# Kernel tuning notes

Hardware: AMD Instinct MI355X
Metric: run time of the kernel (lower is better)

## Reference

```python
import jax, jax.numpy as jnp
import numpy as np

B, T, H = 32, 512, 512
NUM_LAYERS = 2  # outer modules; each nn.GRU itself has NUM_LAYERS internal layers
TOTAL = NUM_LAYERS * NUM_LAYERS  # 4 actual recurrent layers
EPS = 1e-5


def setup_inputs() -> dict:
    key = jax.random.key(0)
    ks = jax.random.split(key, 8)
    s = 1.0 / np.sqrt(H)
    x = jax.random.normal(ks[0], (B, T, H), dtype=jnp.float32)
    # descending lengths in [1, T] (enforce_sorted=True in torch)
    seq_lens = jnp.sort(jax.random.randint(ks[1], (B,), 1, T + 1))[::-1]
    Wih = jax.random.uniform(ks[2], (TOTAL, 3 * H, H), minval=-s, maxval=s)
    Whh = jax.random.uniform(ks[3], (TOTAL, 3 * H, H), minval=-s, maxval=s)
    bih = jax.random.uniform(ks[4], (TOTAL, 3 * H), minval=-s, maxval=s)
    bhh = jax.random.uniform(ks[5], (TOTAL, 3 * H), minval=-s, maxval=s)
    gamma = jnp.ones((NUM_LAYERS, H), jnp.float32)
    beta = jnp.zeros((NUM_LAYERS, H), jnp.float32)
    return {"x": x, "Wih": Wih, "Whh": Whh, "bih": bih, "bhh": bhh,
            "gamma": gamma, "beta": beta, "seq_lens": seq_lens}


def _gru_layer(x, wih, whh, bi, bh):
    # x: [B,T,I]; torch GRU equations (gate order r,z,n)
    xi = jnp.einsum('bti,gi->btg', x, wih) + bi  # [B,T,3H]

    def step(h, xt):
        hh = h @ whh.T + bh
        xr, xz, xn = jnp.split(xt, 3, axis=-1)
        hr, hz, hn = jnp.split(hh, 3, axis=-1)
        r = jax.nn.sigmoid(xr + hr)
        z = jax.nn.sigmoid(xz + hz)
        n = jnp.tanh(xn + r * hn)
        h = (1 - z) * n + z * h
        return h, h

    h0 = jnp.zeros((x.shape[0], whh.shape[1]), x.dtype)
    _, ys = jax.lax.scan(step, h0, jnp.swapaxes(xi, 0, 1))  # [T,B,H]
    return jnp.swapaxes(ys, 0, 1)


def _layernorm(x, g, b):
    mu = jnp.mean(x, axis=-1, keepdims=True)
    var = jnp.mean(jnp.square(x - mu), axis=-1, keepdims=True)
    return (x - mu) * jax.lax.rsqrt(var + EPS) * g + b


def reference(x, Wih, Whh, bih, bhh, gamma, beta, seq_lens):
    # pack_padded_sequence semantics (unidirectional): outputs at valid steps
    # t < len match the full-sequence run; padded steps become zeros after
    # pad_packed_sequence, then LayerNorm is applied to the whole padded tensor.
    mask = (jnp.arange(T)[None, :] < seq_lens[:, None])[:, :, None]  # [B,T,1]
    out = x
    idx = 0
    for l in range(NUM_LAYERS):
        for _k in range(NUM_LAYERS):  # each nn.GRU has NUM_LAYERS internal layers
            out = _gru_layer(out, Wih[idx], Whh[idx], bih[idx], bhh[idx])
            idx += 1
        out = jnp.where(mask, out, 0.0)
        out = _layernorm(out, gamma[l], beta[l])
    return out
```

## Files before the change

### kernel.cpp

```cpp
#include <hip/hip_runtime.h>

typedef unsigned short ushort_t;
typedef __attribute__((ext_vector_type(8))) short short8;
typedef __attribute__((ext_vector_type(4))) float f32x4;

#define B_ 32
#define T_ 512
#define H_ 512
#define CH_ 16

__device__ __forceinline__ float bf2f(ushort_t u) {
  union { unsigned int i; float f; } v; v.i = ((unsigned int)u) << 16; return v.f;
}
__device__ __forceinline__ ushort_t f2bf(float f) {
  union { float fv; unsigned int i; } v; v.fv = f;
  unsigned int x = v.i;
  x += 0x7fffu + ((x >> 16) & 1u);
  return (ushort_t)(x >> 16);
}

__device__ __forceinline__ float fsig(float a) {
  return __builtin_amdgcn_rcpf(1.f + __expf(-a));
}
__device__ __forceinline__ float ftanh(float a) {
  return 1.f - 2.f * __builtin_amdgcn_rcpf(1.f + __expf(2.f * a));
}

__device__ __forceinline__ void cload16(short8& dst, const ushort_t* p) {
  asm volatile("global_load_dwordx4 %0, %1, off sc0 sc1"
               : "=v"(dst) : "v"(p) : "memory");
}
__device__ __forceinline__ void cstore16(const short8& v, ushort_t* p) {
  asm volatile("global_store_dwordx4 %1, %0, off sc0 sc1"
               :: "v"(v), "v"(p) : "memory");
}
#define WAIT_VM0 asm volatile("s_waitcnt vmcnt(0)" ::: "memory")
__device__ __forceinline__ void vfence(short8& v) { asm volatile("" : "+v"(v)); }

__device__ __forceinline__ void poll_row(const int* row, int nf) {
  const int lane = threadIdx.x & 63;
  if (nf > 64) {
    for (;;) {
      int a = __hip_atomic_load(row + lane,      __ATOMIC_RELAXED, __HIP_MEMORY_SCOPE_AGENT);
      int b = __hip_atomic_load(row + 64 + lane, __ATOMIC_RELAXED, __HIP_MEMORY_SCOPE_AGENT);
      if (__all(a != 0 && b != 0)) break;
      __builtin_amdgcn_s_sleep(1);
    }
  } else {
    for (;;) {
      int a = (lane < nf)
            ? __hip_atomic_load(row + lane, __ATOMIC_RELAXED, __HIP_MEMORY_SCOPE_AGENT) : 1;
      if (__all(a != 0)) break;
      __builtin_amdgcn_s_sleep(1);
    }
  }
  asm volatile("" ::: "memory");
}

__global__ void prep_w(const float* __restrict__ Wih, const float* __restrict__ Whh,
                       ushort_t* __restrict__ WihBf, ushort_t* __restrict__ WhhBf) {
  int i = blockIdx.x * 256 + threadIdx.x;
  WihBf[i] = f2bf(Wih[i]);
  WhhBf[i] = f2bf(Whh[i]);
}
__global__ void prep_x(const float* __restrict__ x, ushort_t* __restrict__ xA) {
  int i = blockIdx.x * 256 + threadIdx.x;
  int h  = i & (H_ - 1);
  int tb = i >> 9;
  int b  = tb & (B_ - 1);
  int t  = tb >> 5;
  xA[i] = f2bf(x[((size_t)b * T_ + t) * H_ + h]);
}

__device__ void gru_stage(
    const ushort_t* __restrict__ xin, ushort_t* __restrict__ xout,
    const ushort_t* __restrict__ Wih, const ushort_t* __restrict__ Whh,
    const float* __restrict__ bih, const float* __restrict__ bhh,
    ushort_t* __restrict__ hbuf,
    int* __restrict__ selfFl,
    const int* __restrict__ prodFl,
    int prodN, int wg,
    float (*Gbuf)[2][48][33])
{
  const int tid   = threadIdx.x;
  const int lane  = tid & 63;
  const int wave  = tid >> 6;
  const int jb    = wg * CH_;
  const int m16   = lane & 15;
  const int quad  = lane >> 4;
  const int bcol  = (wave & 1) * 16 + m16;

  const ushort_t* Wsel = (wave < 2) ? Wih : Whh;
  short8 afrag[3][16];
#pragma unroll
  for (int g = 0; g < 3; ++g) {
    const ushort_t* wp = Wsel + (size_t)(g * H_ + jb + m16) * H_ + quad * 8;
#pragma unroll
    for (int kk = 0; kk < 16; ++kk)
      afrag[g][kk] = *(const short8*)(wp + kk * 32);
  }

  const int b0 = tid & 31;
  const int c  = tid >> 5;
  const int c0 = 2 * c, c1 = 2 * c + 1;
  const float bxr0 = bih[0*H_ + jb + c0], bhr0 = bhh[0*H_ + jb + c0];
  const float bxz0 = bih[1*H_ + jb + c0], bhz0 = bhh[1*H_ + jb + c0];
  const float bxn0 = bih[2*H_ + jb + c0], bhn0 = bhh[2*H_ + jb + c0];
  const float bxr1 = bih[0*H_ + jb + c1], bhr1 = bhh[0*H_ + jb + c1];
  const float bxz1 = bih[1*H_ + jb + c1], bhz1 = bhh[1*H_ + jb + c1];
  const float bxn1 = bih[2*H_ + jb + c1], bhn1 = bhh[2*H_ + jb + c1];
  float hp0 = 0.f, hp1 = 0.f;

  for (int s = 0; s < T_; ++s) {
    const int p = s & 1;
    f32x4 acc0 = {0.f, 0.f, 0.f, 0.f};
    f32x4 acc1 = acc0, acc2 = acc0;

    if (wave < 2) {
      const ushort_t* src = xin + ((size_t)s * B_ + bcol) * H_ + quad * 8;
      if (prodFl) {
        poll_row(prodFl + s * prodN, prodN);
        short8 bfr[16];
#pragma unroll
        for (int kk = 0; kk < 16; ++kk) cload16(bfr[kk], src + kk * 32);
        WAIT_VM0;
#pragma unroll
        for (int kk = 0; kk < 16; ++kk) {
          vfence(bfr[kk]);
          acc0 = __builtin_amdgcn_mfma_f32_16x16x32_bf16(afrag[0][kk], bfr[kk], acc0, 0, 0, 0);
          acc1 = __builtin_amdgcn_mfma_f32_16x16x32_bf16(afrag[1][kk], bfr[kk], acc1, 0, 0, 0);
          acc2 = __builtin_amdgcn_mfma_f32_16x16x32_bf16(afrag[2][kk], bfr[kk], acc2, 0, 0, 0);
        }
      } else {
#pragma unroll
        for (int kk = 0; kk < 16; ++kk) {
          short8 bf = *(const short8*)(src + kk * 32);
          acc0 = __builtin_amdgcn_mfma_f32_16x16x32_bf16(afrag[0][kk], bf, acc0, 0, 0, 0);
          acc1 = __builtin_amdgcn_mfma_f32_16x16x32_bf16(afrag[1][kk], bf, acc1, 0, 0, 0);
          acc2 = __builtin_amdgcn_mfma_f32_16x16x32_bf16(afrag[2][kk], bf, acc2, 0, 0, 0);
        }
      }
    } else {
      if (s > 0) poll_row(selfFl + (s - 1) * 128, 128);
      const ushort_t* src = hbuf + ((size_t)p * B_ + bcol) * H_ + quad * 8;
      short8 bfr[16];
#pragma unroll
      for (int kk = 0; kk < 16; ++kk) cload16(bfr[kk], src + kk * 32);
      WAIT_VM0;
#pragma unroll
      for (int kk = 0; kk < 16; ++kk) {
        vfence(bfr[kk]);
        acc0 = __builtin_amdgcn_mfma_f32_16x16x32_bf16(afrag[0][kk], bfr[kk], acc0, 0, 0, 0);
        acc1 = __builtin_amdgcn_mfma_f32_16x16x32_bf16(afrag[1][kk], bfr[kk], acc1, 0, 0, 0);
        acc2 = __builtin_amdgcn_mfma_f32_16x16x32_bf16(afrag[2][kk], bfr[kk], acc2, 0, 0, 0);
      }
    }

    float (*Gd)[33] = Gbuf[p][(wave < 2) ? 0 : 1];
#pragma unroll
    for (int r = 0; r < 4; ++r) {
      Gd[ 0 + quad * 4 + r][bcol] = acc0[r];
      Gd[16 + quad * 4 + r][bcol] = acc1[r];
      Gd[32 + quad * 4 + r][bcol] = acc2[r];
    }
    __syncthreads();

    float (*Gx)[33] = Gbuf[p][0];
    float (*Gh)[33] = Gbuf[p][1];
    ushort_t* hdst = hbuf + (size_t)(p ^ 1) * B_ * H_;
    {
      float rr = fsig(Gx[c0][b0] + bxr0 + Gh[c0][b0] + bhr0);
      float zz = fsig(Gx[16 + c0][b0] + bxz0 + Gh[16 + c0][b0] + bhz0);
      float nn = ftanh(Gx[32 + c0][b0] + bxn0 + rr * (Gh[32 + c0][b0] + bhn0));
      hp0 = (1.f - zz) * nn + zz * hp0;
    }
    {
      float rr = fsig(Gx[c1][b0] + bxr1 + Gh[c1][b0] + bhr1);
      float zz = fsig(Gx[16 + c1][b0] + bxz1 + Gh[16 + c1][b0] + bhz1);
      float nn = ftanh(Gx[32 + c1][b0] + bxn1 + rr * (Gh[32 + c1][b0] + bhn1));
      hp1 = (1.f - zz) * nn + zz * hp1;
    }
    unsigned int pack = (unsigned int)f2bf(hp0) | ((unsigned int)f2bf(hp1) << 16);
    __hip_atomic_store((unsigned int*)(hdst + (size_t)b0 * H_ + jb + c0), pack,
                       __ATOMIC_RELAXED, __HIP_MEMORY_SCOPE_AGENT);
    __hip_atomic_store((unsigned int*)(xout + ((size_t)s * B_ + b0) * H_ + jb + c0), pack,
                       __ATOMIC_RELAXED, __HIP_MEMORY_SCOPE_AGENT);

    WAIT_VM0;
    if (lane == 0)
      __hip_atomic_store(selfFl + s * 128 + wg * 4 + wave, 1,
                         __ATOMIC_RELAXED, __HIP_MEMORY_SCOPE_AGENT);
  }
}

__device__ void ln_stage(
    const ushort_t* __restrict__ xin,
    ushort_t* __restrict__ xout_bf,
    float* __restrict__ out_f32,
    const float* __restrict__ gamma, const float* __restrict__ beta,
    const int* __restrict__ seq,
    int* __restrict__ selfFl,
    const int* __restrict__ prodFl, int prodN, int wg)
{
  const int lane = threadIdx.x & 63;
  const int wv   = threadIdx.x >> 6;
  const int b    = wg * 4 + wv;
  const int len  = seq[b];
  const int h0   = lane * 8;

  float g[8], be[8];
#pragma unroll
  for (int j = 0; j < 8; ++j) { g[j] = gamma[h0 + j]; be[j] = beta[h0 + j]; }

  for (int s = 0; s < T_; ++s) {
    poll_row(prodFl + s * prodN, prodN);
    short8 raw;
    cload16(raw, xin + ((size_t)s * B_ + b) * H_ + h0);
    WAIT_VM0;
    vfence(raw);
    const bool valid = s < len;
    float v[8];
#pragma unroll
    for (int j = 0; j < 8; ++j) v[j] = valid ? bf2f((ushort_t)raw[j]) : 0.f;

    float sum = 0.f, sq = 0.f;
#pragma unroll
    for (int j = 0; j < 8; ++j) { sum += v[j]; sq += v[j] * v[j]; }
#pragma unroll
    for (int off = 32; off > 0; off >>= 1) {
      sum += __shfl_xor(sum, off);
      sq  += __shfl_xor(sq, off);
    }
    float mu   = sum * (1.f / H_);
    float var  = sq * (1.f / H_) - mu * mu;
    float rstd = rsqrtf(var + 1e-5f);

    if (xout_bf) {
      short8 o;
#pragma unroll
      for (int j = 0; j < 8; ++j)
        o[j] = (short)f2bf((v[j] - mu) * rstd * g[j] + be[j]);
      cstore16(o, xout_bf + ((size_t)s * B_ + b) * H_ + h0);
      WAIT_VM0;
      if (lane == 0)
        __hip_atomic_store(selfFl + s * 32 + b, 1,
                           __ATOMIC_RELAXED, __HIP_MEMORY_SCOPE_AGENT);
    } else {
      float* dst = out_f32 + ((size_t)b * T_ + s) * H_ + h0;
#pragma unroll
      for (int j = 0; j < 8; ++j)
        dst[j] = (v[j] - mu) * rstd * g[j] + be[j];
    }
  }
}

__global__ __launch_bounds__(256, 1) void gru_mega(
    ushort_t* __restrict__ xA, ushort_t* __restrict__ xB, ushort_t* __restrict__ xC,
    const ushort_t* __restrict__ WihBf, const ushort_t* __restrict__ WhhBf,
    const float* __restrict__ bih, const float* __restrict__ bhh,
    const float* __restrict__ gamma, const float* __restrict__ beta,
    const int* __restrict__ seq,
    ushort_t* __restrict__ hbase, int* __restrict__ flbase,
    float* __restrict__ out)
{
  __shared__ float Gbuf[2][2][48][33];

  const int bid = blockIdx.x;
  const int GRUF = T_ * 128;
  const int LNF  = T_ * 32;
  int* fl0   = flbase;
  int* fl1   = flbase + GRUF;
  int* flln0 = flbase + 2 * GRUF;
  int* fl2   = flbase + 2 * GRUF + LNF;
  int* fl3   = flbase + 3 * GRUF + LNF;
  const int WM  = 3 * H_ * H_;
  const int HBL = 2 * B_ * H_;

  if (bid < 32) {
    gru_stage(xA, xB, WihBf, WhhBf, bih, bhh,
              hbase, fl0, nullptr, 0, bid, Gbuf);
  } else if (bid < 64) {
    gru_stage(xB, xC, WihBf + WM, WhhBf + WM, bih + 1536, bhh + 1536,
              hbase + HBL, fl1, fl0, 128, bid - 32, Gbuf);
  } else if (bid < 72) {
    ln_stage(xC, xA, nullptr, gamma, beta, seq, flln0, fl1, 128, bid - 64);
  } else if (bid < 104) {
    gru_stage(xA, xC, WihBf + 2 * WM, WhhBf + 2 * WM, bih + 2 * 1536, bhh + 2 * 1536,
              hbase + 2 * HBL, fl2, flln0, 32, bid - 72, Gbuf);
  } else if (bid < 136) {
    gru_stage(xC, xB, WihBf + 3 * WM, WhhBf + 3 * WM, bih + 3 * 1536, bhh + 3 * 1536,
              hbase + 3 * HBL, fl3, fl2, 128, bid - 104, Gbuf);
  } else {
    ln_stage(xB, nullptr, out, gamma + H_, beta + H_, seq,
             nullptr, fl3, 128, bid - 136);
  }
}

#define WIH_OFF 0u
#define WHH_OFF 6291456u
#define XA_OFF  12582912u
#define XB_OFF  29360128u
#define XC_OFF  46137344u
#define HB_OFF  62914560u
#define FL_OFF  63176704u

extern "C" void kernel_launch(void* const* d_in, const int* in_sizes, int n_in,
                              void* d_out, int out_size, void* d_ws, size_t ws_size,
                              hipStream_t stream) {
  (void)in_sizes; (void)n_in; (void)out_size; (void)ws_size;
  const float* x     = (const float*)d_in[0];
  const float* Wih   = (const float*)d_in[1];
  const float* Whh   = (const float*)d_in[2];
  const float* bih   = (const float*)d_in[3];
  const float* bhh   = (const float*)d_in[4];
  const float* gamma = (const float*)d_in[5];
  const float* beta  = (const float*)d_in[6];
  const int*   seq   = (const int*)d_in[7];

  char* ws = (char*)d_ws;
  ushort_t* WihBf = (ushort_t*)(ws + WIH_OFF);
  ushort_t* WhhBf = (ushort_t*)(ws + WHH_OFF);
  ushort_t* xA    = (ushort_t*)(ws + XA_OFF);
  ushort_t* xB    = (ushort_t*)(ws + XB_OFF);
  ushort_t* xC    = (ushort_t*)(ws + XC_OFF);
  ushort_t* hbase = (ushort_t*)(ws + HB_OFF);
  int*      flags = (int*)(ws + FL_OFF);

  hipMemsetAsync(ws + HB_OFF, 0, 262144u + 1114112u, stream);

  prep_w<<<3145728 / 256, 256, 0, stream>>>(Wih, Whh, WihBf, WhhBf);
  prep_x<<<8388608 / 256, 256, 0, stream>>>(x, xA);

  gru_mega<<<144, 256, 0, stream>>>(xA, xB, xC, WihBf, WhhBf,
                                    bih, bhh, gamma, beta, seq,
                                    hbase, flags, (float*)d_out);
}
```

Measured before the change: 3.891 ms.

## Tag hidden-state words with step index and tile activations per workgroup

Each hidden-state value is stored as a 32-bit word carrying the bf16 value plus a step tag. Consumers spin-read the h buffer until every tag reaches the current step, so the recurrent wait no longer depends only on flag arrays plus a full store fence. Activations are re-laid out in per-workgroup 16-column tiles so MFMA operand loads are contiguous, and separate x/h flag arrays let flags be published with partial vmcnt waits instead of vmcnt(0). This adds doubled h traffic and a polling loop over 32 loads per step, and the still-present hFl poll may cancel part of the latency saved.

Result: slower. 4.537 ms (+16.6%).

```diff
diff --git a/kernel.cpp b/kernel.cpp
--- a/kernel.cpp
+++ b/kernel.cpp
@@ -1,13 +1,15 @@
 #include <hip/hip_runtime.h>
 
 typedef unsigned short ushort_t;
+typedef unsigned int uint_t;
 typedef __attribute__((ext_vector_type(8))) short short8;
 typedef __attribute__((ext_vector_type(4))) float f32x4;
+typedef __attribute__((ext_vector_type(4))) unsigned int u32x4;
 
 #define B_ 32
 #define T_ 512
 #define H_ 512
-#define CH_ 16
+#define XT_ 16384
 
 __device__ __forceinline__ float bf2f(ushort_t u) {
   union { unsigned int i; float f; } v; v.i = ((unsigned int)u) << 16; return v.f;
@@ -18,6 +20,7 @@
   x += 0x7fffu + ((x >> 16) & 1u);
   return (ushort_t)(x >> 16);
 }
+__device__ __forceinline__ uint_t umin_(uint_t a, uint_t b) { return a < b ? a : b; }
 
 __device__ __forceinline__ float fsig(float a) {
   return __builtin_amdgcn_rcpf(1.f + __expf(-a));
@@ -26,15 +29,24 @@
   return 1.f - 2.f * __builtin_amdgcn_rcpf(1.f + __expf(2.f * a));
 }
 
-__device__ __forceinline__ void cload16(short8& dst, const ushort_t* p) {
-  asm volatile("global_load_dwordx4 %0, %1, off sc0 sc1"
-               : "=v"(dst) : "v"(p) : "memory");
+__device__ __forceinline__ void cload16(short8& d, const ushort_t* p) {
+  asm volatile("global_load_dwordx4 %0, %1, off sc0 sc1" : "=v"(d) : "v"(p) : "memory");
+}
+__device__ __forceinline__ void cload16u(u32x4& d, const uint_t* p) {
+  asm volatile("global_load_dwordx4 %0, %1, off sc0 sc1" : "=v"(d) : "v"(p) : "memory");
 }
 __device__ __forceinline__ void cstore16(const short8& v, ushort_t* p) {
-  asm volatile("global_store_dwordx4 %1, %0, off sc0 sc1"
-               :: "v"(v), "v"(p) : "memory");
+  asm volatile("global_store_dwordx4 %1, %0, off sc0 sc1" :: "v"(v), "v"(p) : "memory");
+}
+__device__ __forceinline__ void cstore8(unsigned long long v, uint_t* p) {
+  asm volatile("global_store_dwordx2 %1, %0, off sc0 sc1" :: "v"(v), "v"(p) : "memory");
+}
+__device__ __forceinline__ void cstore4(uint_t v, ushort_t* p) {
+  asm volatile("global_store_dword %1, %0, off sc0 sc1" :: "v"(v), "v"(p) : "memory");
 }
 #define WAIT_VM0 asm volatile("s_waitcnt vmcnt(0)" ::: "memory")
+#define WAIT_VM1 asm volatile("s_waitcnt vmcnt(1)" ::: "memory")
+#define WAIT_VM3 asm volatile("s_waitcnt vmcnt(3)" ::: "memory")
 __device__ __forceinline__ void vfence(short8& v) { asm volatile("" : "+v"(v)); }
 
 __device__ __forceinline__ void poll_row(const int* row, int nf) {
@@ -65,19 +77,20 @@
 }
 __global__ void prep_x(const float* __restrict__ x, ushort_t* __restrict__ xA) {
   int i = blockIdx.x * 256 + threadIdx.x;
-  int h  = i & (H_ - 1);
-  int tb = i >> 9;
-  int b  = tb & (B_ - 1);
-  int t  = tb >> 5;
-  xA[i] = f2bf(x[((size_t)b * T_ + t) * H_ + h]);
+  int ch = i & 15;
+  int b  = (i >> 4) & 31;
+  int wg = (i >> 9) & 31;
+  int t  = i >> 14;
+  xA[i] = f2bf(x[((size_t)b * T_ + t) * H_ + wg * 16 + ch]);
 }
 
 __device__ void gru_stage(
     const ushort_t* __restrict__ xin, ushort_t* __restrict__ xout,
     const ushort_t* __restrict__ Wih, const ushort_t* __restrict__ Whh,
     const float* __restrict__ bih, const float* __restrict__ bhh,
-    ushort_t* __restrict__ hbuf,
-    int* __restrict__ selfFl,
+    uint_t* __restrict__ hT,
+    int* __restrict__ xFl,
+    int* __restrict__ hFl,
     const int* __restrict__ prodFl,
     int prodN, int wg,
     float (*Gbuf)[2][48][33])
@@ -85,7 +98,7 @@
   const int tid   = threadIdx.x;
   const int lane  = tid & 63;
   const int wave  = tid >> 6;
-  const int jb    = wg * CH_;
+  const int jb    = wg * 16;
   const int m16   = lane & 15;
   const int quad  = lane >> 4;
   const int bcol  = (wave & 1) * 16 + m16;
@@ -100,9 +113,9 @@
       afrag[g][kk] = *(const short8*)(wp + kk * 32);
   }
 
-  const int b0 = tid & 31;
-  const int c  = tid >> 5;
-  const int c0 = 2 * c, c1 = 2 * c + 1;
+  const int b0 = tid >> 3;
+  const int c8 = tid & 7;
+  const int c0 = 2 * c8, c1 = c0 + 1;
   const float bxr0 = bih[0*H_ + jb + c0], bhr0 = bhh[0*H_ + jb + c0];
   const float bxz0 = bih[1*H_ + jb + c0], bhz0 = bhh[1*H_ + jb + c0];
   const float bxn0 = bih[2*H_ + jb + c0], bhn0 = bhh[2*H_ + jb + c0];
@@ -111,18 +124,21 @@
   const float bxn1 = bih[2*H_ + jb + c1], bhn1 = bhh[2*H_ + jb + c1];
   float hp0 = 0.f, hp1 = 0.f;
 
+  const int xoff = (quad >> 1) * 512 + bcol * 16 + (quad & 1) * 8;
+  const uint_t* hb = hT + (quad >> 1) * 512 + bcol * 16 + (quad & 1) * 8;
+
   for (int s = 0; s < T_; ++s) {
     const int p = s & 1;
     f32x4 acc0 = {0.f, 0.f, 0.f, 0.f};
     f32x4 acc1 = acc0, acc2 = acc0;
 
     if (wave < 2) {
-      const ushort_t* src = xin + ((size_t)s * B_ + bcol) * H_ + quad * 8;
+      const ushort_t* src = xin + (size_t)s * XT_ + xoff;
       if (prodFl) {
         poll_row(prodFl + s * prodN, prodN);
         short8 bfr[16];
 #pragma unroll
-        for (int kk = 0; kk < 16; ++kk) cload16(bfr[kk], src + kk * 32);
+        for (int kk = 0; kk < 16; ++kk) cload16(bfr[kk], src + kk * 1024);
         WAIT_VM0;
 #pragma unroll
         for (int kk = 0; kk < 16; ++kk) {
@@ -134,25 +150,39 @@
       } else {
 #pragma unroll
         for (int kk = 0; kk < 16; ++kk) {
-          short8 bf = *(const short8*)(src + kk * 32);
+          short8 bf = *(const short8*)(src + kk * 1024);
           acc0 = __builtin_amdgcn_mfma_f32_16x16x32_bf16(afrag[0][kk], bf, acc0, 0, 0, 0);
           acc1 = __builtin_amdgcn_mfma_f32_16x16x32_bf16(afrag[1][kk], bf, acc1, 0, 0, 0);
           acc2 = __builtin_amdgcn_mfma_f32_16x16x32_bf16(afrag[2][kk], bf, acc2, 0, 0, 0);
         }
       }
-    } else {
-      if (s > 0) poll_row(selfFl + (s - 1) * 128, 128);
-      const ushort_t* src = hbuf + ((size_t)p * B_ + bcol) * H_ + quad * 8;
-      short8 bfr[16];
-#pragma unroll
-      for (int kk = 0; kk < 16; ++kk) cload16(bfr[kk], src + kk * 32);
-      WAIT_VM0;
+    } else if (s > 0) {
+      poll_row(hFl + (s - 1) * 128, 128);
+      const uint_t* hsrc = hb + p * 16384;
+      const uint_t tgt = ((uint_t)s) << 16;
+      u32x4 t[32];
+      for (;;) {
+#pragma unroll
+        for (int i = 0; i < 32; ++i)
+          cload16u(t[i], hsrc + (i >> 1) * 1024 + (i & 1) * 4);
+        WAIT_VM0;
+        uint_t m = 0xffffffffu;
+#pragma unroll
+        for (int i = 0; i < 32; ++i)
+          m = umin_(m, umin_(umin_(t[i].x, t[i].y), umin_(t[i].z, t[i].w)));
+        if (__all(m >= tgt)) break;
+        __builtin_amdgcn_s_sleep(2);
+      }
 #pragma unroll
       for (int kk = 0; kk < 16; ++kk) {
-        vfence(bfr[kk]);
-        acc0 = __builtin_amdgcn_mfma_f32_16x16x32_bf16(afrag[0][kk], bfr[kk], acc0, 0, 0, 0);
-        acc1 = __builtin_amdgcn_mfma_f32_16x16x32_bf16(afrag[1][kk], bfr[kk], acc1, 0, 0, 0);
-        acc2 = __builtin_amdgcn_mfma_f32_16x16x32_bf16(afrag[2][kk], bfr[kk], acc2, 0, 0, 0);
+        union { uint_t w[4]; short8 v; } u;
+        u.w[0] = __builtin_amdgcn_perm(t[2*kk].y,   t[2*kk].x,   0x05040100u);
+        u.w[1] = __builtin_amdgcn_perm(t[2*kk].w,   t[2*kk].z,   0x05040100u);
+        u.w[2] = __builtin_amdgcn_perm(t[2*kk+1].y, t[2*kk+1].x, 0x05040100u);
+        u.w[3] = __builtin_amdgcn_perm(t[2*kk+1].w, t[2*kk+1].z, 0x05040100u);
+        acc0 = __builtin_amdgcn_mfma_f32_16x16x32_bf16(afrag[0][kk], u.v, acc0, 0, 0, 0);
+        acc1 = __builtin_amdgcn_mfma_f32_16x16x32_bf16(afrag[1][kk], u.v, acc1, 0, 0, 0);
+        acc2 = __builtin_amdgcn_mfma_f32_16x16x32_bf16(afrag[2][kk], u.v, acc2, 0, 0, 0);
       }
     }
 
@@ -167,7 +197,6 @@
 
     float (*Gx)[33] = Gbuf[p][0];
     float (*Gh)[33] = Gbuf[p][1];
-    ushort_t* hdst = hbuf + (size_t)(p ^ 1) * B_ * H_;
     {
       float rr = fsig(Gx[c0][b0] + bxr0 + Gh[c0][b0] + bhr0);
       float zz = fsig(Gx[16 + c0][b0] + bxz0 + Gh[16 + c0][b0] + bhz0);
@@ -180,17 +209,24 @@
       float nn = ftanh(Gx[32 + c1][b0] + bxn1 + rr * (Gh[32 + c1][b0] + bhn1));
       hp1 = (1.f - zz) * nn + zz * hp1;
     }
-    unsigned int pack = (unsigned int)f2bf(hp0) | ((unsigned int)f2bf(hp1) << 16);
-    __hip_atomic_store((unsigned int*)(hdst + (size_t)b0 * H_ + jb + c0), pack,
+    const uint_t tagv = (uint_t)(s + 1);
+    uint_t v0 = (uint_t)f2bf(hp0), v1 = (uint_t)f2bf(hp1);
+    unsigned long long hw = (unsigned long long)(v0 | (tagv << 16))
+                          | ((unsigned long long)(v1 | (tagv << 16)) << 32);
+    cstore8(hw, hT + ((s + 1) & 1) * 16384 + wg * 512 + b0 * 16 + c0);
+    cstore4(v0 | (v1 << 16), xout + (size_t)s * XT_ + wg * 512 + b0 * 16 + c0);
+    if (lane == 0)
+      __hip_atomic_store(hFl + s * 128 + wg * 4 + wave, 1,
+                         __ATOMIC_RELAXED, __HIP_MEMORY_SCOPE_AGENT);
+    WAIT_VM3;
+    if (s > 0 && lane == 0)
+      __hip_atomic_store(xFl + (s - 1) * 128 + wg * 4 + wave, 1,
+                         __ATOMIC_RELAXED, __HIP_MEMORY_SCOPE_AGENT);
+  }
+  WAIT_VM0;
+  if (lane == 0)
+    __hip_atomic_store(xFl + (T_ - 1) * 128 + wg * 4 + wave, 1,
                        __ATOMIC_RELAXED, __HIP_MEMORY_SCOPE_AGENT);
-    __hip_atomic_store((unsigned int*)(xout + ((size_t)s * B_ + b0) * H_ + jb + c0), pack,
-                       __ATOMIC_RELAXED, __HIP_MEMORY_SCOPE_AGENT);
-
-    WAIT_VM0;
-    if (lane == 0)
-      __hip_atomic_store(selfFl + s * 128 + wg * 4 + wave, 1,
-                         __ATOMIC_RELAXED, __HIP_MEMORY_SCOPE_AGENT);
-  }
 }
 
 __device__ void ln_stage(
@@ -206,6 +242,7 @@
   const int wv   = threadIdx.x >> 6;
   const int b    = wg * 4 + wv;
   const int len  = seq[b];
+  const int off  = (lane >> 1) * 512 + b * 16 + (lane & 1) * 8;
   const int h0   = lane * 8;
 
   float g[8], be[8];
@@ -215,7 +252,7 @@
   for (int s = 0; s < T_; ++s) {
     poll_row(prodFl + s * prodN, prodN);
     short8 raw;
-    cload16(raw, xin + ((size_t)s * B_ + b) * H_ + h0);
+    cload16(raw, xin + (size_t)s * XT_ + off);
     WAIT_VM0;
     vfence(raw);
     const bool valid = s < len;
@@ -227,23 +264,23 @@
 #pragma unroll
     for (int j = 0; j < 8; ++j) { sum += v[j]; sq += v[j] * v[j]; }
 #pragma unroll
-    for (int off = 32; off > 0; off >>= 1) {
-      sum += __shfl_xor(sum, off);
-      sq  += __shfl_xor(sq, off);
+    for (int o = 32; o > 0; o >>= 1) {
+      sum += __shfl_xor(sum, o);
+      sq  += __shfl_xor(sq, o);
     }
     float mu   = sum * (1.f / H_);
     float var  = sq * (1.f / H_) - mu * mu;
     float rstd = rsqrtf(var + 1e-5f);
 
     if (xout_bf) {
-      short8 o;
+      short8 o8;
 #pragma unroll
       for (int j = 0; j < 8; ++j)
-        o[j] = (short)f2bf((v[j] - mu) * rstd * g[j] + be[j]);
-      cstore16(o, xout_bf + ((size_t)s * B_ + b) * H_ + h0);
-      WAIT_VM0;
-      if (lane == 0)
-        __hip_atomic_store(selfFl + s * 32 + b, 1,
+        o8[j] = (short)f2bf((v[j] - mu) * rstd * g[j] + be[j]);
+      cstore16(o8, xout_bf + (size_t)s * XT_ + off);
+      WAIT_VM1;
+      if (s > 0 && lane == 0)
+        __hip_atomic_store(selfFl + (s - 1) * 32 + b, 1,
                            __ATOMIC_RELAXED, __HIP_MEMORY_SCOPE_AGENT);
     } else {
       float* dst = out_f32 + ((size_t)b * T_ + s) * H_ + h0;
@@ -251,6 +288,12 @@
       for (int j = 0; j < 8; ++j)
         dst[j] = (v[j] - mu) * rstd * g[j] + be[j];
     }
+  }
+  if (xout_bf) {
+    WAIT_VM0;
+    if (lane == 0)
+      __hip_atomic_store(selfFl + (T_ - 1) * 32 + b, 1,
+                         __ATOMIC_RELAXED, __HIP_MEMORY_SCOPE_AGENT);
   }
 }
 
@@ -260,39 +303,38 @@
     const float* __restrict__ bih, const float* __restrict__ bhh,
     const float* __restrict__ gamma, const float* __restrict__ beta,
     const int* __restrict__ seq,
-    ushort_t* __restrict__ hbase, int* __restrict__ flbase,
+    uint_t* __restrict__ hTbase, int* __restrict__ xflbase,
+    int* __restrict__ hflbase, int* __restrict__ lnfl,
     float* __restrict__ out)
 {
   __shared__ float Gbuf[2][2][48][33];
 
   const int bid = blockIdx.x;
-  const int GRUF = T_ * 128;
-  const int LNF  = T_ * 32;
-  int* fl0   = flbase;
-  int* fl1   = flbase + GRUF;
-  int* flln0 = flbase + 2 * GRUF;
-  int* fl2   = flbase + 2 * GRUF + LNF;
-  int* fl3   = flbase + 3 * GRUF + LNF;
-  const int WM  = 3 * H_ * H_;
-  const int HBL = 2 * B_ * H_;
+  const int FS = T_ * 128;
+  const int WM = 3 * H_ * H_;
+  const int HTS = 2 * 32 * 32 * 16;
 
   if (bid < 32) {
     gru_stage(xA, xB, WihBf, WhhBf, bih, bhh,
-              hbase, fl0, nullptr, 0, bid, Gbuf);
+              hTbase, xflbase, hflbase, nullptr, 0, bid, Gbuf);
   } else if (bid < 64) {
     gru_stage(xB, xC, WihBf + WM, WhhBf + WM, bih + 1536, bhh + 1536,
-              hbase + HBL, fl1, fl0, 128, bid - 32, Gbuf);
+              hTbase + HTS, xflbase + FS, hflbase + FS,
+              xflbase, 128, bid - 32, Gbuf);
   } else if (bid < 72) {
-    ln_stage(xC, xA, nullptr, gamma, beta, seq, flln0, fl1, 128, bid - 64);
+    ln_stage(xC, xA, nullptr, gamma, beta, seq, lnfl,
+             xflbase + FS, 128, bid - 64);
   } else if (bid < 104) {
     gru_stage(xA, xC, WihBf + 2 * WM, WhhBf + 2 * WM, bih + 2 * 1536, bhh + 2 * 1536,
-              hbase + 2 * HBL, fl2, flln0, 32, bid - 72, Gbuf);
+              hTbase + 2 * HTS, xflbase + 2 * FS, hflbase + 2 * FS,
+              lnfl, 32, bid - 72, Gbuf);
   } else if (bid < 136) {
     gru_stage(xC, xB, WihBf + 3 * WM, WhhBf + 3 * WM, bih + 3 * 1536, bhh + 3 * 1536,
-              hbase + 3 * HBL, fl3, fl2, 128, bid - 104, Gbuf);
+              hTbase + 3 * HTS, xflbase + 3 * FS, hflbase + 3 * FS,
+              xflbase + 2 * FS, 128, bid - 104, Gbuf);
   } else {
     ln_stage(xB, nullptr, out, gamma + H_, beta + H_, seq,
-             nullptr, fl3, 128, bid - 136);
+             nullptr, xflbase + 3 * FS, 128, bid - 136);
   }
 }
 
@@ -301,8 +343,10 @@
 #define XA_OFF  12582912u
 #define XB_OFF  29360128u
 #define XC_OFF  46137344u
-#define HB_OFF  62914560u
-#define FL_OFF  63176704u
+#define HT_OFF  62914560u
+#define XFL_OFF 63438848u
+#define HFL_OFF 64487424u
+#define LNF_OFF 65536000u
 
 extern "C" void kernel_launch(void* const* d_in, const int* in_sizes, int n_in,
                               void* d_out, int out_size, void* d_ws, size_t ws_size,
@@ -323,15 +367,17 @@
   ushort_t* xA    = (ushort_t*)(ws + XA_OFF);
   ushort_t* xB    = (ushort_t*)(ws + XB_OFF);
   ushort_t* xC    = (ushort_t*)(ws + XC_OFF);
-  ushort_t* hbase = (ushort_t*)(ws + HB_OFF);
-  int*      flags = (int*)(ws + FL_OFF);
-
-  hipMemsetAsync(ws + HB_OFF, 0, 262144u + 1114112u, stream);
-
-  prep_w<<<3145728 / 256, 256, 0, stream>>>(Wih, Whh, WihBf, WhhBf);
-  prep_x<<<8388608 / 256, 256, 0, stream>>>(x, xA);
+  uint_t*   hT    = (uint_t*)(ws + HT_OFF);
+  int*      xfl   = (int*)(ws + XFL_OFF);
+  int*      hfl   = (int*)(ws + HFL_OFF);
+  int*      lnf   = (int*)(ws + LNF_OFF);
+
+  hipMemsetAsync(ws + HT_OFF, 0, 2686976u, stream);
+
+  prep_w<<<12288, 256, 0, stream>>>(Wih, Whh, WihBf, WhhBf);
+  prep_x<<<32768, 256, 0, stream>>>(x, xA);
 
   gru_mega<<<144, 256, 0, stream>>>(xA, xB, xC, WihBf, WhhBf,
                                     bih, bhh, gamma, beta, seq,
-                                    hbase, flags, (float*)d_out);
-}
+                                    hT, xfl, hfl, lnf, (float*)d_out);
+}
```

## Repartition GRU pipeline into 8 wide workgroups per layer with LDS-shared inputs

Applied to the files above, without the earlier changes.

Each GRU layer now runs on 8 workgroups of 1024 threads, each owning 64 hidden units, instead of 32 workgroups of 256 threads owning 16. Only one wave pair per input kind loads the x and h fragments from global memory and shares them through LDS, which cuts redundant global loads per step. Activations are stored in a blocked layout of 64-column tiles to match. Completion flags become bytes polled as packed dwords, and the LayerNorm stages interleave timesteps across two blocks. The cost is extra __syncthreads per step and a larger dynamic LDS footprint, and each block owns more of the per-step gate math.

Result: slower. 13.94 ms (+258.3%).

```diff
diff --git a/kernel.cpp b/kernel.cpp
--- a/kernel.cpp
+++ b/kernel.cpp
@@ -1,13 +1,15 @@
 #include <hip/hip_runtime.h>
 
 typedef unsigned short ushort_t;
+typedef unsigned int uint_t;
 typedef __attribute__((ext_vector_type(8))) short short8;
 typedef __attribute__((ext_vector_type(4))) float f32x4;
+typedef __attribute__((ext_vector_type(4))) float float4_t;
 
 #define B_ 32
 #define T_ 512
 #define H_ 512
-#define CH_ 16
+#define XT_ 16384
 
 __device__ __forceinline__ float bf2f(ushort_t u) {
   union { unsigned int i; float f; } v; v.i = ((unsigned int)u) << 16; return v.f;
@@ -26,33 +28,30 @@
   return 1.f - 2.f * __builtin_amdgcn_rcpf(1.f + __expf(2.f * a));
 }
 
-__device__ __forceinline__ void cload16(short8& dst, const ushort_t* p) {
-  asm volatile("global_load_dwordx4 %0, %1, off sc0 sc1"
-               : "=v"(dst) : "v"(p) : "memory");
+__device__ __forceinline__ void cload16(short8& d, const ushort_t* p) {
+  asm volatile("global_load_dwordx4 %0, %1, off sc0 sc1" : "=v"(d) : "v"(p) : "memory");
+}
+__device__ __forceinline__ void cstore4(uint_t v, ushort_t* p) {
+  asm volatile("global_store_dword %1, %0, off sc0 sc1" :: "v"(v), "v"(p) : "memory");
 }
 __device__ __forceinline__ void cstore16(const short8& v, ushort_t* p) {
-  asm volatile("global_store_dwordx4 %1, %0, off sc0 sc1"
-               :: "v"(v), "v"(p) : "memory");
+  asm volatile("global_store_dwordx4 %1, %0, off sc0 sc1" :: "v"(v), "v"(p) : "memory");
+}
+__device__ __forceinline__ void cstoreb(unsigned char* p) {
+  asm volatile("global_store_byte %0, %1, off sc0 sc1" :: "v"(p), "v"(1) : "memory");
 }
 #define WAIT_VM0 asm volatile("s_waitcnt vmcnt(0)" ::: "memory")
 __device__ __forceinline__ void vfence(short8& v) { asm volatile("" : "+v"(v)); }
 
-__device__ __forceinline__ void poll_row(const int* row, int nf) {
+__device__ __forceinline__ void poll_bytes(const unsigned char* row, int n4) {
   const int lane = threadIdx.x & 63;
-  if (nf > 64) {
-    for (;;) {
-      int a = __hip_atomic_load(row + lane,      __ATOMIC_RELAXED, __HIP_MEMORY_SCOPE_AGENT);
-      int b = __hip_atomic_load(row + 64 + lane, __ATOMIC_RELAXED, __HIP_MEMORY_SCOPE_AGENT);
-      if (__all(a != 0 && b != 0)) break;
-      __builtin_amdgcn_s_sleep(1);
-    }
-  } else {
-    for (;;) {
-      int a = (lane < nf)
-            ? __hip_atomic_load(row + lane, __ATOMIC_RELAXED, __HIP_MEMORY_SCOPE_AGENT) : 1;
-      if (__all(a != 0)) break;
-      __builtin_amdgcn_s_sleep(1);
-    }
+  const uint_t* r = (const uint_t*)row;
+  for (;;) {
+    uint_t a = (lane < n4)
+             ? __hip_atomic_load(r + lane, __ATOMIC_RELAXED, __HIP_MEMORY_SCOPE_AGENT)
+             : 0x01010101u;
+    if (__all(a == 0x01010101u)) break;
+    __builtin_amdgcn_s_sleep(1);
   }
   asm volatile("" ::: "memory");
 }
@@ -65,11 +64,11 @@
 }
 __global__ void prep_x(const float* __restrict__ x, ushort_t* __restrict__ xA) {
   int i = blockIdx.x * 256 + threadIdx.x;
-  int h  = i & (H_ - 1);
-  int tb = i >> 9;
-  int b  = tb & (B_ - 1);
-  int t  = tb >> 5;
-  xA[i] = f2bf(x[((size_t)b * T_ + t) * H_ + h]);
+  int ch = i & 63;
+  int b  = (i >> 6) & 31;
+  int wg = (i >> 11) & 7;
+  int t  = i >> 14;
+  xA[i] = f2bf(x[((size_t)b * T_ + t) * H_ + wg * 64 + ch]);
 }
 
 __device__ void gru_stage(
@@ -77,32 +76,39 @@
     const ushort_t* __restrict__ Wih, const ushort_t* __restrict__ Whh,
     const float* __restrict__ bih, const float* __restrict__ bhh,
     ushort_t* __restrict__ hbuf,
-    int* __restrict__ selfFl,
-    const int* __restrict__ prodFl,
-    int prodN, int wg,
-    float (*Gbuf)[2][48][33])
+    unsigned char* __restrict__ selfFl,
+    const unsigned char* __restrict__ inFl,
+    int inN4, int wg, char* lds)
 {
-  const int tid   = threadIdx.x;
-  const int lane  = tid & 63;
-  const int wave  = tid >> 6;
-  const int jb    = wg * CH_;
-  const int m16   = lane & 15;
-  const int quad  = lane >> 4;
-  const int bcol  = (wave & 1) * 16 + m16;
-
-  const ushort_t* Wsel = (wave < 2) ? Wih : Whh;
+  const int tid  = threadIdx.x;
+  const int lane = tid & 63;
+  const int wave = tid >> 6;
+  const int isH  = wave >> 3;
+  const int wl   = wave & 7;
+  const int ct   = wl >> 1, bh = wl & 1;
+  const bool loader = (ct == 0);
+  const int m16  = lane & 15, quad = lane >> 4;
+  const int jb   = wg * 64;
+
+  const ushort_t* Wsel = isH ? Whh : Wih;
   short8 afrag[3][16];
 #pragma unroll
   for (int g = 0; g < 3; ++g) {
-    const ushort_t* wp = Wsel + (size_t)(g * H_ + jb + m16) * H_ + quad * 8;
+    const ushort_t* wp = Wsel + (size_t)(g * H_ + jb + ct * 16 + m16) * H_ + quad * 8;
 #pragma unroll
     for (int kk = 0; kk < 16; ++kk)
       afrag[g][kk] = *(const short8*)(wp + kk * 32);
   }
 
-  const int b0 = tid & 31;
-  const int c  = tid >> 5;
-  const int c0 = 2 * c, c1 = 2 * c + 1;
+  char* stage = lds + isH * 32768;
+  float* Gx = (float*)(lds + 65536);
+  float* Gh = Gx + 192 * 33;
+  float* Gmine = isH ? Gh : Gx;
+  const int fragoff = (bh * 1024 + quad * 16 + m16) * 16;
+  const int colbase = (bh * 16 + m16) * 64 + quad * 8;
+
+  const int b0 = tid >> 5;
+  const int c0 = (tid & 31) * 2, c1 = c0 + 1;
   const float bxr0 = bih[0*H_ + jb + c0], bhr0 = bhh[0*H_ + jb + c0];
   const float bxz0 = bih[1*H_ + jb + c0], bhz0 = bhh[1*H_ + jb + c0];
   const float bxn0 = bih[2*H_ + jb + c0], bhn0 = bhh[2*H_ + jb + c0];
@@ -112,21 +118,47 @@
   float hp0 = 0.f, hp1 = 0.f;
 
   for (int s = 0; s < T_; ++s) {
-    const int p = s & 1;
     f32x4 acc0 = {0.f, 0.f, 0.f, 0.f};
     f32x4 acc1 = acc0, acc2 = acc0;
-
-    if (wave < 2) {
-      const ushort_t* src = xin + ((size_t)s * B_ + bcol) * H_ + quad * 8;
-      if (prodFl) {
-        poll_row(prodFl + s * prodN, prodN);
-        short8 bfr[16];
-#pragma unroll
-        for (int kk = 0; kk < 16; ++kk) cload16(bfr[kk], src + kk * 32);
+    short8 bfr[16];
+    const bool active = !isH || (s > 0);
+
+    if (active && loader) {
+      if (!isH) {
+        const ushort_t* src = xin + (size_t)s * XT_ + colbase;
+        if (inFl) {
+          poll_bytes(inFl + (size_t)s * inN4 * 4, inN4);
+#pragma unroll
+          for (int kk = 0; kk < 16; ++kk)
+            cload16(bfr[kk], src + (kk >> 1) * 2048 + (kk & 1) * 32);
+          WAIT_VM0;
+#pragma unroll
+          for (int kk = 0; kk < 16; ++kk) vfence(bfr[kk]);
+        } else {
+#pragma unroll
+          for (int kk = 0; kk < 16; ++kk)
+            bfr[kk] = *(const short8*)(src + (kk >> 1) * 2048 + (kk & 1) * 32);
+        }
+      } else {
+        poll_bytes(selfFl + (size_t)(s - 1) * 128, 32);
+        const ushort_t* src = hbuf + (size_t)(s & 1) * XT_ + colbase;
+#pragma unroll
+        for (int kk = 0; kk < 16; ++kk)
+          cload16(bfr[kk], src + (kk >> 1) * 2048 + (kk & 1) * 32);
         WAIT_VM0;
 #pragma unroll
+        for (int kk = 0; kk < 16; ++kk) vfence(bfr[kk]);
+      }
+#pragma unroll
+      for (int kk = 0; kk < 16; ++kk)
+        *(short8*)(stage + fragoff + kk * 1024) = bfr[kk];
+    }
+    __syncthreads();
+
+    if (active) {
+      if (loader) {
+#pragma unroll
         for (int kk = 0; kk < 16; ++kk) {
-          vfence(bfr[kk]);
           acc0 = __builtin_amdgcn_mfma_f32_16x16x32_bf16(afrag[0][kk], bfr[kk], acc0, 0, 0, 0);
           acc1 = __builtin_amdgcn_mfma_f32_16x16x32_bf16(afrag[1][kk], bfr[kk], acc1, 0, 0, 0);
           acc2 = __builtin_amdgcn_mfma_f32_16x16x32_bf16(afrag[2][kk], bfr[kk], acc2, 0, 0, 0);
@@ -134,62 +166,43 @@
       } else {
 #pragma unroll
         for (int kk = 0; kk < 16; ++kk) {
-          short8 bf = *(const short8*)(src + kk * 32);
-          acc0 = __builtin_amdgcn_mfma_f32_16x16x32_bf16(afrag[0][kk], bf, acc0, 0, 0, 0);
-          acc1 = __builtin_amdgcn_mfma_f32_16x16x32_bf16(afrag[1][kk], bf, acc1, 0, 0, 0);
-          acc2 = __builtin_amdgcn_mfma_f32_16x16x32_bf16(afrag[2][kk], bf, acc2, 0, 0, 0);
+          short8 fr = *(const short8*)(stage + fragoff + kk * 1024);
+          acc0 = __builtin_amdgcn_mfma_f32_16x16x32_bf16(afrag[0][kk], fr, acc0, 0, 0, 0);
+          acc1 = __builtin_amdgcn_mfma_f32_16x16x32_bf16(afrag[1][kk], fr, acc1, 0, 0, 0);
+          acc2 = __builtin_amdgcn_mfma_f32_16x16x32_bf16(afrag[2][kk], fr, acc2, 0, 0, 0);
         }
       }
-    } else {
-      if (s > 0) poll_row(selfFl + (s - 1) * 128, 128);
-      const ushort_t* src = hbuf + ((size_t)p * B_ + bcol) * H_ + quad * 8;
-      short8 bfr[16];
-#pragma unroll
-      for (int kk = 0; kk < 16; ++kk) cload16(bfr[kk], src + kk * 32);
-      WAIT_VM0;
-#pragma unroll
-      for (int kk = 0; kk < 16; ++kk) {
-        vfence(bfr[kk]);
-        acc0 = __builtin_amdgcn_mfma_f32_16x16x32_bf16(afrag[0][kk], bfr[kk], acc0, 0, 0, 0);
-        acc1 = __builtin_amdgcn_mfma_f32_16x16x32_bf16(afrag[1][kk], bfr[kk], acc1, 0, 0, 0);
-        acc2 = __builtin_amdgcn_mfma_f32_16x16x32_bf16(afrag[2][kk], bfr[kk], acc2, 0, 0, 0);
-      }
-    }
-
-    float (*Gd)[33] = Gbuf[p][(wave < 2) ? 0 : 1];
-#pragma unroll
-    for (int r = 0; r < 4; ++r) {
-      Gd[ 0 + quad * 4 + r][bcol] = acc0[r];
-      Gd[16 + quad * 4 + r][bcol] = acc1[r];
-      Gd[32 + quad * 4 + r][bcol] = acc2[r];
+    }
+
+    {
+      const int col = bh * 16 + m16;
+#pragma unroll
+      for (int r = 0; r < 4; ++r) {
+        Gmine[(  0 + ct * 16 + quad * 4 + r) * 33 + col] = acc0[r];
+        Gmine[( 64 + ct * 16 + quad * 4 + r) * 33 + col] = acc1[r];
+        Gmine[(128 + ct * 16 + quad * 4 + r) * 33 + col] = acc2[r];
+      }
     }
     __syncthreads();
 
-    float (*Gx)[33] = Gbuf[p][0];
-    float (*Gh)[33] = Gbuf[p][1];
-    ushort_t* hdst = hbuf + (size_t)(p ^ 1) * B_ * H_;
     {
-      float rr = fsig(Gx[c0][b0] + bxr0 + Gh[c0][b0] + bhr0);
-      float zz = fsig(Gx[16 + c0][b0] + bxz0 + Gh[16 + c0][b0] + bhz0);
-      float nn = ftanh(Gx[32 + c0][b0] + bxn0 + rr * (Gh[32 + c0][b0] + bhn0));
+      float rr = fsig(Gx[(  0 + c0) * 33 + b0] + bxr0 + Gh[(  0 + c0) * 33 + b0] + bhr0);
+      float zz = fsig(Gx[( 64 + c0) * 33 + b0] + bxz0 + Gh[( 64 + c0) * 33 + b0] + bhz0);
+      float nn = ftanh(Gx[(128 + c0) * 33 + b0] + bxn0 + rr * (Gh[(128 + c0) * 33 + b0] + bhn0));
       hp0 = (1.f - zz) * nn + zz * hp0;
     }
     {
-      float rr = fsig(Gx[c1][b0] + bxr1 + Gh[c1][b0] + bhr1);
-      float zz = fsig(Gx[16 + c1][b0] + bxz1 + Gh[16 + c1][b0] + bhz1);
-      float nn = ftanh(Gx[32 + c1][b0] + bxn1 + rr * (Gh[32 + c1][b0] + bhn1));
+      float rr = fsig(Gx[(  0 + c1) * 33 + b0] + bxr1 + Gh[(  0 + c1) * 33 + b0] + bhr1);
+      float zz = fsig(Gx[( 64 + c1) * 33 + b0] + bxz1 + Gh[( 64 + c1) * 33 + b0] + bhz1);
+      float nn = ftanh(Gx[(128 + c1) * 33 + b0] + bxn1 + rr * (Gh[(128 + c1) * 33 + b0] + bhn1));
       hp1 = (1.f - zz) * nn + zz * hp1;
     }
-    unsigned int pack = (unsigned int)f2bf(hp0) | ((unsigned int)f2bf(hp1) << 16);
-    __hip_atomic_store((unsigned int*)(hdst + (size_t)b0 * H_ + jb + c0), pack,
-                       __ATOMIC_RELAXED, __HIP_MEMORY_SCOPE_AGENT);
-    __hip_atomic_store((unsigned int*)(xout + ((size_t)s * B_ + b0) * H_ + jb + c0), pack,
-                       __ATOMIC_RELAXED, __HIP_MEMORY_SCOPE_AGENT);
-
+    uint_t pack = (uint_t)f2bf(hp0) | ((uint_t)f2bf(hp1) << 16);
+    cstore4(pack, hbuf + (size_t)((s + 1) & 1) * XT_ + wg * 2048 + b0 * 64 + c0);
+    cstore4(pack, xout + (size_t)s * XT_ + wg * 2048 + b0 * 64 + c0);
     WAIT_VM0;
     if (lane == 0)
-      __hip_atomic_store(selfFl + s * 128 + wg * 4 + wave, 1,
-                         __ATOMIC_RELAXED, __HIP_MEMORY_SCOPE_AGENT);
+      cstoreb(selfFl + (size_t)s * 128 + wg * 16 + wave);
   }
 }
 
@@ -199,100 +212,100 @@
     float* __restrict__ out_f32,
     const float* __restrict__ gamma, const float* __restrict__ beta,
     const int* __restrict__ seq,
-    int* __restrict__ selfFl,
-    const int* __restrict__ prodFl, int prodN, int wg)
+    unsigned char* __restrict__ selfFl,
+    const unsigned char* __restrict__ prodFl, int prodN4, int par)
 {
   const int lane = threadIdx.x & 63;
   const int wv   = threadIdx.x >> 6;
-  const int b    = wg * 4 + wv;
-  const int len  = seq[b];
-  const int h0   = lane * 8;
+  const int r0 = wv, r1 = wv + 16;
+  const int len0 = seq[r0], len1 = seq[r1];
+  const int off  = (lane >> 3) * 2048 + (lane & 7) * 8;
 
   float g[8], be[8];
 #pragma unroll
-  for (int j = 0; j < 8; ++j) { g[j] = gamma[h0 + j]; be[j] = beta[h0 + j]; }
-
-  for (int s = 0; s < T_; ++s) {
-    poll_row(prodFl + s * prodN, prodN);
-    short8 raw;
-    cload16(raw, xin + ((size_t)s * B_ + b) * H_ + h0);
+  for (int j = 0; j < 8; ++j) { g[j] = gamma[lane * 8 + j]; be[j] = beta[lane * 8 + j]; }
+
+  for (int s = par; s < T_; s += 2) {
+    poll_bytes(prodFl + (size_t)s * prodN4 * 4, prodN4);
+    short8 raw0, raw1;
+    cload16(raw0, xin + (size_t)s * XT_ + off + r0 * 64);
+    cload16(raw1, xin + (size_t)s * XT_ + off + r1 * 64);
     WAIT_VM0;
-    vfence(raw);
-    const bool valid = s < len;
-    float v[8];
-#pragma unroll
-    for (int j = 0; j < 8; ++j) v[j] = valid ? bf2f((ushort_t)raw[j]) : 0.f;
-
-    float sum = 0.f, sq = 0.f;
-#pragma unroll
-    for (int j = 0; j < 8; ++j) { sum += v[j]; sq += v[j] * v[j]; }
-#pragma unroll
-    for (int off = 32; off > 0; off >>= 1) {
-      sum += __shfl_xor(sum, off);
-      sq  += __shfl_xor(sq, off);
-    }
-    float mu   = sum * (1.f / H_);
-    float var  = sq * (1.f / H_) - mu * mu;
-    float rstd = rsqrtf(var + 1e-5f);
-
-    if (xout_bf) {
-      short8 o;
-#pragma unroll
-      for (int j = 0; j < 8; ++j)
-        o[j] = (short)f2bf((v[j] - mu) * rstd * g[j] + be[j]);
-      cstore16(o, xout_bf + ((size_t)s * B_ + b) * H_ + h0);
+    vfence(raw0); vfence(raw1);
+
+#pragma unroll
+    for (int rr = 0; rr < 2; ++rr) {
+      const short8& raw = rr ? raw1 : raw0;
+      const int r = rr ? r1 : r0;
+      const bool valid = s < (rr ? len1 : len0);
+      float v[8];
+#pragma unroll
+      for (int j = 0; j < 8; ++j) v[j] = valid ? bf2f((ushort_t)raw[j]) : 0.f;
+      float sum = 0.f, sq = 0.f;
+#pragma unroll
+      for (int j = 0; j < 8; ++j) { sum += v[j]; sq += v[j] * v[j]; }
+#pragma unroll
+      for (int o = 32; o > 0; o >>= 1) {
+        sum += __shfl_xor(sum, o);
+        sq  += __shfl_xor(sq, o);
+      }
+      float mu   = sum * (1.f / H_);
+      float var  = sq * (1.f / H_) - mu * mu;
+      float rstd = rsqrtf(var + 1e-5f);
+      if (xout_bf) {
+        short8 o8;
+#pragma unroll
+        for (int j = 0; j < 8; ++j)
+          o8[j] = (short)f2bf((v[j] - mu) * rstd * g[j] + be[j]);
+        cstore16(o8, xout_bf + (size_t)s * XT_ + off + r * 64);
+      } else {
+        float* dst = out_f32 + ((size_t)r * T_ + s) * H_ + lane * 8;
+        float4_t o4a, o4b;
+#pragma unroll
+        for (int j = 0; j < 4; ++j) o4a[j] = (v[j] - mu) * rstd * g[j] + be[j];
+#pragma unroll
+        for (int j = 0; j < 4; ++j) o4b[j] = (v[4 + j] - mu) * rstd * g[4 + j] + be[4 + j];
+        *(float4_t*)dst = o4a;
+        *(float4_t*)(dst + 4) = o4b;
+      }
+    }
+    if (selfFl) {
       WAIT_VM0;
-      if (lane == 0)
-        __hip_atomic_store(selfFl + s * 32 + b, 1,
-                           __ATOMIC_RELAXED, __HIP_MEMORY_SCOPE_AGENT);
-    } else {
-      float* dst = out_f32 + ((size_t)b * T_ + s) * H_ + h0;
-#pragma unroll
-      for (int j = 0; j < 8; ++j)
-        dst[j] = (v[j] - mu) * rstd * g[j] + be[j];
-    }
-  }
-}
-
-__global__ __launch_bounds__(256, 1) void gru_mega(
+      if (lane == 0) cstoreb(selfFl + (size_t)s * 16 + wv);
+    }
+  }
+}
+
+__global__ __launch_bounds__(1024) void gru_mega(
     ushort_t* __restrict__ xA, ushort_t* __restrict__ xB, ushort_t* __restrict__ xC,
     const ushort_t* __restrict__ WihBf, const ushort_t* __restrict__ WhhBf,
     const float* __restrict__ bih, const float* __restrict__ bhh,
     const float* __restrict__ gamma, const float* __restrict__ beta,
     const int* __restrict__ seq,
-    ushort_t* __restrict__ hbase, int* __restrict__ flbase,
-    float* __restrict__ out)
+    ushort_t* __restrict__ hbase, unsigned char* __restrict__ gfl,
+    unsigned char* __restrict__ lnfl, float* __restrict__ out)
 {
-  __shared__ float Gbuf[2][2][48][33];
-
+  extern __shared__ char lds[];
   const int bid = blockIdx.x;
-  const int GRUF = T_ * 128;
-  const int LNF  = T_ * 32;
-  int* fl0   = flbase;
-  int* fl1   = flbase + GRUF;
-  int* flln0 = flbase + 2 * GRUF;
-  int* fl2   = flbase + 2 * GRUF + LNF;
-  int* fl3   = flbase + 3 * GRUF + LNF;
-  const int WM  = 3 * H_ * H_;
-  const int HBL = 2 * B_ * H_;
+  const int WM = 3 * H_ * H_;
+  const int FL = T_ * 128;
 
   if (bid < 32) {
-    gru_stage(xA, xB, WihBf, WhhBf, bih, bhh,
-              hbase, fl0, nullptr, 0, bid, Gbuf);
-  } else if (bid < 64) {
-    gru_stage(xB, xC, WihBf + WM, WhhBf + WM, bih + 1536, bhh + 1536,
-              hbase + HBL, fl1, fl0, 128, bid - 32, Gbuf);
-  } else if (bid < 72) {
-    ln_stage(xC, xA, nullptr, gamma, beta, seq, flln0, fl1, 128, bid - 64);
-  } else if (bid < 104) {
-    gru_stage(xA, xC, WihBf + 2 * WM, WhhBf + 2 * WM, bih + 2 * 1536, bhh + 2 * 1536,
-              hbase + 2 * HBL, fl2, flln0, 32, bid - 72, Gbuf);
-  } else if (bid < 136) {
-    gru_stage(xC, xB, WihBf + 3 * WM, WhhBf + 3 * WM, bih + 3 * 1536, bhh + 3 * 1536,
-              hbase + 3 * HBL, fl3, fl2, 128, bid - 104, Gbuf);
+    const int layer = bid >> 3, wg = bid & 7;
+    const ushort_t* xi; ushort_t* xo;
+    const unsigned char* inFl; int inN4;
+    if (layer == 0)      { xi = xA; xo = xB; inFl = nullptr;      inN4 = 0;  }
+    else if (layer == 1) { xi = xB; xo = xC; inFl = gfl;          inN4 = 32; }
+    else if (layer == 2) { xi = xA; xo = xC; inFl = lnfl;         inN4 = 4;  }
+    else                 { xi = xC; xo = xB; inFl = gfl + 2 * FL; inN4 = 32; }
+    gru_stage(xi, xo, WihBf + layer * WM, WhhBf + layer * WM,
+              bih + layer * 1536, bhh + layer * 1536,
+              hbase + layer * 2 * XT_, gfl + layer * FL, inFl, inN4, wg, lds);
+  } else if (bid < 34) {
+    ln_stage(xC, xA, nullptr, gamma, beta, seq, lnfl, gfl + 1 * FL, 32, bid - 32);
   } else {
     ln_stage(xB, nullptr, out, gamma + H_, beta + H_, seq,
-             nullptr, fl3, 128, bid - 136);
+             nullptr, gfl + 3 * FL, 32, bid - 34);
   }
 }
 
@@ -302,7 +315,9 @@
 #define XB_OFF  29360128u
 #define XC_OFF  46137344u
 #define HB_OFF  62914560u
-#define FL_OFF  63176704u
+#define GFL_OFF 63176704u
+#define LNF_OFF 63438848u
+#define LDS_BYTES 116224
 
 extern "C" void kernel_launch(void* const* d_in, const int* in_sizes, int n_in,
                               void* d_out, int out_size, void* d_ws, size_t ws_size,
@@ -324,14 +339,21 @@
   ushort_t* xB    = (ushort_t*)(ws + XB_OFF);
   ushort_t* xC    = (ushort_t*)(ws + XC_OFF);
   ushort_t* hbase = (ushort_t*)(ws + HB_OFF);
-  int*      flags = (int*)(ws + FL_OFF);
-
-  hipMemsetAsync(ws + HB_OFF, 0, 262144u + 1114112u, stream);
-
-  prep_w<<<3145728 / 256, 256, 0, stream>>>(Wih, Whh, WihBf, WhhBf);
-  prep_x<<<8388608 / 256, 256, 0, stream>>>(x, xA);
-
-  gru_mega<<<144, 256, 0, stream>>>(xA, xB, xC, WihBf, WhhBf,
-                                    bih, bhh, gamma, beta, seq,
-                                    hbase, flags, (float*)d_out);
-}
+  unsigned char* gfl  = (unsigned char*)(ws + GFL_OFF);
+  unsigned char* lnf  = (unsigned char*)(ws + LNF_OFF);
+
+  hipMemsetAsync(ws + HB_OFF, 0, 532480u, stream);
+
+  prep_w<<<12288, 256, 0, stream>>>(Wih, Whh, WihBf, WhhBf);
+  prep_x<<<32768, 256, 0, stream>>>(x, xA);
+
+  static int lds_set = 0;
+  if (!lds_set) {
+    hipFuncSetAttribute((const void*)gru_mega,
+                        hipFuncAttributeMaxDynamicSharedMemorySize, LDS_BYTES);
+    lds_set = 1;
+  }
+  gru_mega<<<36, 1024, LDS_BYTES, stream>>>(xA, xB, xC, WihBf, WhhBf,
+                                            bih, bhh, gamma, beta, seq,
+                                            hbase, gfl, lnf, (float*)d_out);
+}
```
